# Kernel optimization log

Measured on AMD Instinct MI355X. Metric: run time of the kernel, lower is better.

The kernel has to match this reference:

```python
import jax, jax.numpy as jnp
import numpy as np

MAX_LANES = 5
DELTA_V = 1.0
DELTA_D = 6.0


def setup_inputs() -> dict:
    key = jax.random.key(0)
    k1, k2 = jax.random.split(key)
    targets = jax.random.randint(k1, (32, 360, 640), 0, 6, dtype=jnp.int32)
    embedding_vector = jax.random.normal(k2, (32, 4, 360, 640), dtype=jnp.float32)
    return {"targets": targets, "embedding_vector": embedding_vector}


def reference(targets, embedding_vector):
    B, C, H, W = embedding_vector.shape
    L = MAX_LANES
    P = H * W
    t = targets.reshape(B, P)                      # [B,P] labels 0..L
    e = embedding_vector.reshape(B, C, P)          # [B,C,P]

    # per-(batch, lane) segment counts and means
    onehot = (t[:, None, :] == jnp.arange(1, L + 1, dtype=t.dtype)[None, :, None])  # [B,L,P]
    counts = onehot.sum(-1)                        # [B,L] int
    valid = counts > 1                             # lane used only if >1 points
    sums = jnp.einsum('blp,bcp->blc', onehot.astype(e.dtype), e)   # [B,L,C]
    means = sums / jnp.maximum(counts, 1)[..., None].astype(e.dtype)  # [B,L,C]

    # ---- variance (pull) loss: per-point distance to its lane mean ----
    means_ext = jnp.concatenate([jnp.zeros((B, 1, C), e.dtype), means], axis=1)  # [B,L+1,C]
    mean_pix = jnp.take_along_axis(means_ext, t[..., None].astype(jnp.int32), axis=1)  # [B,P,C]
    diff = e.transpose(0, 2, 1) - mean_pix         # [B,P,C]
    sq = jnp.sum(diff * diff, axis=-1)             # [B,P]
    dist = jnp.sqrt(jnp.maximum(sq, 1e-12))
    valid_ext = jnp.concatenate([jnp.zeros((B, 1), bool), valid], axis=1)  # [B,L+1]
    pix_valid = jnp.take_along_axis(valid_ext, t.astype(jnp.int32), axis=1)  # [B,P]
    hinge = jax.nn.relu(dist - DELTA_V)
    dist_sum = jnp.sum(jnp.where(pix_valid, hinge * hinge, 0.0))
    point_count = jnp.sum(jnp.where(valid, counts, 0)).astype(e.dtype)
    dist_loss = jnp.where(point_count > 0, dist_sum / jnp.maximum(point_count, 1.0), 0.0)

    # ---- distance (push) loss: pdist over valid lane means per batch ----
    d = means[:, :, None, :] - means[:, None, :, :]          # [B,L,L,C]
    psq = jnp.sum(d * d, axis=-1)                            # [B,L,L]
    pd = jnp.sqrt(jnp.maximum(psq, 1e-12))
    iu = jnp.arange(L)
    pair_mask = valid[:, :, None] & valid[:, None, :] & (iu[:, None] < iu[None, :])  # [B,L,L]
    ph = jax.nn.relu(DELTA_D - pd)
    per_batch_sum = jnp.sum(jnp.where(pair_mask, ph * ph, 0.0), axis=(1, 2))  # [B]
    npairs = pair_mask.sum((1, 2)).astype(e.dtype)           # [B]
    batch_has = npairs > 0                                   # needs >=2 valid lanes
    var_b = jnp.where(batch_has, per_batch_sum / jnp.maximum(npairs, 1.0), 0.0)
    n_batches = batch_has.sum().astype(e.dtype)
    var_loss = jnp.where(n_batches > 0, var_b.sum() / jnp.maximum(n_batches, 1.0), 0.0)

    return dist_loss + var_loss
```

## Files before the change

### kernel.cpp

```cpp
#include <hip/hip_runtime.h>
#include <math.h>

#define B 32
#define C 4
#define H 360
#define W 640
#define P (H*W)
#define L 5
#define DELTA_V 1.0f
#define DELTA_D 6.0f

#define NV 25
#define BLK1 64
#define NBLK (B*BLK1)
#define G4 (P/4)

__device__ __forceinline__ float waveReduce(float v) {
#pragma unroll
    for (int off = 32; off; off >>= 1) v += __shfl_down(v, off, 64);
    return v;
}

__global__ __launch_bounds__(256) void seg_sums_k(const int* __restrict__ tgt,
                                                  const float* __restrict__ emb,
                                                  float* __restrict__ part1) {
    const int b = blockIdx.y;
    float s[L][C];
    float cn[L];
#pragma unroll
    for (int l = 0; l < L; ++l) {
        cn[l] = 0.f;
#pragma unroll
        for (int c = 0; c < C; ++c) s[l][c] = 0.f;
    }

    const int4*   t4 = (const int4*)(tgt + (size_t)b * P);
    const float4* e0 = (const float4*)(emb + (size_t)(b*C + 0) * P);
    const float4* e1 = (const float4*)(emb + (size_t)(b*C + 1) * P);
    const float4* e2 = (const float4*)(emb + (size_t)(b*C + 2) * P);
    const float4* e3 = (const float4*)(emb + (size_t)(b*C + 3) * P);

    auto proc = [&](int tt, float x0, float x1, float x2, float x3) {
#pragma unroll
        for (int l = 0; l < L; ++l) {
            float m = (tt == l + 1) ? 1.0f : 0.0f;
            cn[l] += m;
            s[l][0] = fmaf(m, x0, s[l][0]);
            s[l][1] = fmaf(m, x1, s[l][1]);
            s[l][2] = fmaf(m, x2, s[l][2]);
            s[l][3] = fmaf(m, x3, s[l][3]);
        }
    };

    for (int g = blockIdx.x * 256 + threadIdx.x; g < G4; g += BLK1 * 256) {
        int4   t  = t4[g];
        float4 a0 = e0[g], a1 = e1[g], a2 = e2[g], a3 = e3[g];
        proc(t.x, a0.x, a1.x, a2.x, a3.x);
        proc(t.y, a0.y, a1.y, a2.y, a3.y);
        proc(t.z, a0.z, a1.z, a2.z, a3.z);
        proc(t.w, a0.w, a1.w, a2.w, a3.w);
    }

    float vals[NV];
#pragma unroll
    for (int l = 0; l < L; ++l) {
#pragma unroll
        for (int c = 0; c < C; ++c) vals[l*4 + c] = s[l][c];
        vals[20 + l] = cn[l];
    }

    __shared__ float red[4][NV];
    const int lane = threadIdx.x & 63, wave = threadIdx.x >> 6;
#pragma unroll
    for (int k = 0; k < NV; ++k) {
        float r = waveReduce(vals[k]);
        if (lane == 0) red[wave][k] = r;
    }
    __syncthreads();
    if (threadIdx.x < NV) {
        float r = red[0][threadIdx.x] + red[1][threadIdx.x]
                + red[2][threadIdx.x] + red[3][threadIdx.x];
        part1[(size_t)(b * BLK1 + blockIdx.x) * NV + threadIdx.x] = r;
    }
}

__global__ __launch_bounds__(256) void means_k(const float* __restrict__ part1,
                                               float* __restrict__ means,
                                               float* __restrict__ validf,
                                               float* __restrict__ cntv) {
    const int seg  = (blockIdx.x * 256 + threadIdx.x) >> 6;
    const int lane = threadIdx.x & 63;
    if (seg >= B * L) return;
    const int b = seg / L, l = seg % L;

    const float* p = part1 + (size_t)(b * BLK1 + lane) * NV;
    float v0 = p[l*4+0], v1 = p[l*4+1], v2 = p[l*4+2], v3 = p[l*4+3], vc = p[20+l];
    v0 = waveReduce(v0); v1 = waveReduce(v1); v2 = waveReduce(v2);
    v3 = waveReduce(v3); vc = waveReduce(vc);
    if (lane == 0) {
        const float inv = 1.0f / fmaxf(vc, 1.0f);
        const bool  v   = vc > 1.5f;
        means[seg*4+0] = v0 * inv;
        means[seg*4+1] = v1 * inv;
        means[seg*4+2] = v2 * inv;
        means[seg*4+3] = v3 * inv;
        validf[seg] = v ? 1.f : 0.f;
        cntv[seg]   = v ? vc  : 0.f;
    }
}

__global__ __launch_bounds__(256) void pull_k(const int* __restrict__ tgt,
                                              const float* __restrict__ emb,
                                              const float* __restrict__ means,
                                              const float* __restrict__ validf,
                                              float* __restrict__ part3) {
    __shared__ float4 lmean[L + 1];
    __shared__ float  lvalid[L + 1];
    __shared__ float  lred[4];
    const int b = blockIdx.y;
    const int tid = threadIdx.x;

    if (tid == 0) { lmean[0] = make_float4(0.f, 0.f, 0.f, 0.f); lvalid[0] = 0.f; }
    else if (tid <= L) {
        lmean[tid]  = *(const float4*)(means + ((size_t)b*L + (tid-1)) * C);
        lvalid[tid] = validf[b*L + (tid-1)];
    }
    __syncthreads();

    const int4*   t4 = (const int4*)(tgt + (size_t)b * P);
    const float4* e0 = (const float4*)(emb + (size_t)(b*C + 0) * P);
    const float4* e1 = (const float4*)(emb + (size_t)(b*C + 1) * P);
    const float4* e2 = (const float4*)(emb + (size_t)(b*C + 2) * P);
    const float4* e3 = (const float4*)(emb + (size_t)(b*C + 3) * P);

    float acc = 0.f;
    auto proc = [&](int tt, float x0, float x1, float x2, float x3) {
        float4 m = lmean[tt];
        float d0 = x0 - m.x, d1 = x1 - m.y, d2 = x2 - m.z, d3 = x3 - m.w;
        float sq   = d0*d0 + d1*d1 + d2*d2 + d3*d3;
        float dist = sqrtf(fmaxf(sq, 1e-12f));
        float h    = fmaxf(dist - DELTA_V, 0.f);
        acc = fmaf(lvalid[tt] * h, h, acc);
    };

    for (int g = blockIdx.x * 256 + threadIdx.x; g < G4; g += BLK1 * 256) {
        int4   t  = t4[g];
        float4 a0 = e0[g], a1 = e1[g], a2 = e2[g], a3 = e3[g];
        proc(t.x, a0.x, a1.x, a2.x, a3.x);
        proc(t.y, a0.y, a1.y, a2.y, a3.y);
        proc(t.z, a0.z, a1.z, a2.z, a3.z);
        proc(t.w, a0.w, a1.w, a2.w, a3.w);
    }

    float r = waveReduce(acc);
    const int lane = tid & 63, wave = tid >> 6;
    if (lane == 0) lred[wave] = r;
    __syncthreads();
    if (tid == 0)
        part3[b * BLK1 + blockIdx.x] = lred[0] + lred[1] + lred[2] + lred[3];
}

__global__ __launch_bounds__(256) void finish_k(const float* __restrict__ part3,
                                                const float* __restrict__ means,
                                                const float* __restrict__ validf,
                                                const float* __restrict__ cntv,
                                                float* __restrict__ out) {
    __shared__ float red[4][4];
    const int tid = threadIdx.x;
    const int lane = tid & 63, wave = tid >> 6;

    float vb = 0.f, has = 0.f;
    if (tid < B) {
        const float* mb = means  + tid * L * 4;
        const float* vv = validf + tid * L;
        float ssum = 0.f, np = 0.f;
#pragma unroll
        for (int i = 0; i < L; ++i)
#pragma unroll
            for (int j = i + 1; j < L; ++j) {
                float ok = vv[i] * vv[j];
                float d0 = mb[i*4+0] - mb[j*4+0];
                float d1 = mb[i*4+1] - mb[j*4+1];
                float d2 = mb[i*4+2] - mb[j*4+2];
                float d3 = mb[i*4+3] - mb[j*4+3];
                float psq = d0*d0 + d1*d1 + d2*d2 + d3*d3;
                float pd  = sqrtf(fmaxf(psq, 1e-12f));
                float ph  = fmaxf(DELTA_D - pd, 0.f);
                ssum += ok * ph * ph;
                np   += ok;
            }
        if (np > 0.f) { vb = ssum / np; has = 1.f; }
    }
    float pc = (tid < B*L) ? cntv[tid] : 0.f;
    float ps = 0.f;
    for (int i = tid; i < NBLK; i += 256) ps += part3[i];

    float rvb = waveReduce(vb);
    float rhs = waveReduce(has);
    float rpc = waveReduce(pc);
    float rps = waveReduce(ps);
    if (lane == 0) { red[wave][0]=rvb; red[wave][1]=rhs; red[wave][2]=rpc; red[wave][3]=rps; }
    __syncthreads();
    if (tid == 0) {
        float svb = red[0][0]+red[1][0]+red[2][0]+red[3][0];
        float shs = red[0][1]+red[1][1]+red[2][1]+red[3][1];
        float spc = red[0][2]+red[1][2]+red[2][2]+red[3][2];
        float sps = red[0][3]+red[1][3]+red[2][3]+red[3][3];
        float var = (shs > 0.f) ? svb / shs : 0.f;
        float dl  = (spc > 0.f) ? sps / fmaxf(spc, 1.f) : 0.f;
        out[0] = dl + var;
    }
}

extern "C" void kernel_launch(void* const* d_in, const int* in_sizes, int n_in,
                              void* d_out, int out_size, void* d_ws, size_t ws_size,
                              hipStream_t stream) {
    const int*   tgt = (const int*)d_in[0];
    const float* emb = (const float*)d_in[1];

    float* ws     = (float*)d_ws;
    float* part1  = ws;
    float* means  = part1 + (size_t)NBLK * NV;
    float* validf = means + B*L*C;
    float* cntv   = validf + B*L;
    float* part3  = cntv + B*L;

    dim3 grid(BLK1, B);
    seg_sums_k<<<grid, 256, 0, stream>>>(tgt, emb, part1);
    means_k<<<(B*L + 3) / 4, 256, 0, stream>>>(part1, means, validf, cntv);
    pull_k<<<grid, 256, 0, stream>>>(tgt, emb, means, validf, part3);
    finish_k<<<1, 256, 0, stream>>>(part3, means, validf, cntv, (float*)d_out);
}
```

Measured before the change: 226.0 us.

## Use contiguous per-block chunks with register double-buffered prefetch in both streaming kernels

Each block now handles one contiguous chunk of the image instead of a grid-strided range, and the grid drops to 30 blocks per batch. Loads are software-pipelined through three register stages so the next tiles are in flight while the current one is processed, and a masked tail stage covers the remainder. The launch bounds ask for 4 blocks per SM. The intent is more memory-level parallelism in the bandwidth-bound passes, at the cost of higher register pressure and fewer blocks overall.

```diff
diff --git a/kernel.cpp b/kernel.cpp
--- a/kernel.cpp
+++ b/kernel.cpp
@@ -3,17 +3,17 @@
 
 #define B 32
 #define C 4
-#define H 360
-#define W 640
-#define P (H*W)
+#define P (360*640)
 #define L 5
 #define DELTA_V 1.0f
 #define DELTA_D 6.0f
 
 #define NV 25
-#define BLK1 64
+#define BLK1 30
 #define NBLK (B*BLK1)
 #define G4 (P/4)
+#define CHUNK_G (G4/BLK1)
+#define ITERS ((CHUNK_G + 255)/256)
 
 __device__ __forceinline__ float waveReduce(float v) {
 #pragma unroll
@@ -21,18 +21,14 @@
     return v;
 }
 
-__global__ __launch_bounds__(256) void seg_sums_k(const int* __restrict__ tgt,
-                                                  const float* __restrict__ emb,
-                                                  float* __restrict__ part1) {
-    const int b = blockIdx.y;
-    float s[L][C];
-    float cn[L];
-#pragma unroll
-    for (int l = 0; l < L; ++l) {
-        cn[l] = 0.f;
-#pragma unroll
-        for (int c = 0; c < C; ++c) s[l][c] = 0.f;
-    }
+struct Stage { int4 t; float4 a0, a1, a2, a3; };
+
+__global__ __launch_bounds__(256, 4) void seg_sums_k(const int* __restrict__ tgt,
+                                                     const float* __restrict__ emb,
+                                                     float* __restrict__ part1) {
+    const int b   = blockIdx.y;
+    const int tid = threadIdx.x;
+    const int gbase = blockIdx.x * CHUNK_G;
 
     const int4*   t4 = (const int4*)(tgt + (size_t)b * P);
     const float4* e0 = (const float4*)(emb + (size_t)(b*C + 0) * P);
@@ -40,7 +36,29 @@
     const float4* e2 = (const float4*)(emb + (size_t)(b*C + 2) * P);
     const float4* e3 = (const float4*)(emb + (size_t)(b*C + 3) * P);
 
-    auto proc = [&](int tt, float x0, float x1, float x2, float x3) {
+    float s[L][C], cn[L];
+#pragma unroll
+    for (int l = 0; l < L; ++l) { cn[l]=0.f; s[l][0]=s[l][1]=s[l][2]=s[l][3]=0.f; }
+
+    auto load_full = [&](int it) {
+        Stage st;
+        const int g = gbase + it*256 + tid;
+        st.t = t4[g];
+        st.a0 = e0[g]; st.a1 = e1[g]; st.a2 = e2[g]; st.a3 = e3[g];
+        return st;
+    };
+    auto load_tail = [&](int it) {
+        Stage st;
+        const int off = it*256 + tid;
+        const bool v  = off < CHUNK_G;
+        const int g   = gbase + (v ? off : 0);
+        st.t = t4[g];
+        st.a0 = e0[g]; st.a1 = e1[g]; st.a2 = e2[g]; st.a3 = e3[g];
+        if (!v) { st.t.x = 0; st.t.y = 0; st.t.z = 0; st.t.w = 0; }
+        return st;
+    };
+
+    auto proc1 = [&](int tt, float x0, float x1, float x2, float x3) {
 #pragma unroll
         for (int l = 0; l < L; ++l) {
             float m = (tt == l + 1) ? 1.0f : 0.0f;
@@ -51,15 +69,25 @@
             s[l][3] = fmaf(m, x3, s[l][3]);
         }
     };
-
-    for (int g = blockIdx.x * 256 + threadIdx.x; g < G4; g += BLK1 * 256) {
-        int4   t  = t4[g];
-        float4 a0 = e0[g], a1 = e1[g], a2 = e2[g], a3 = e3[g];
-        proc(t.x, a0.x, a1.x, a2.x, a3.x);
-        proc(t.y, a0.y, a1.y, a2.y, a3.y);
-        proc(t.z, a0.z, a1.z, a2.z, a3.z);
-        proc(t.w, a0.w, a1.w, a2.w, a3.w);
-    }
+    auto procS = [&](const Stage& st) {
+        proc1(st.t.x, st.a0.x, st.a1.x, st.a2.x, st.a3.x);
+        proc1(st.t.y, st.a0.y, st.a1.y, st.a2.y, st.a3.y);
+        proc1(st.t.z, st.a0.z, st.a1.z, st.a2.z, st.a3.z);
+        proc1(st.t.w, st.a0.w, st.a1.w, st.a2.w, st.a3.w);
+    };
+
+    Stage sA = load_full(0);
+    Stage sB = load_full(1);
+#pragma unroll
+    for (int it = 0; it < ITERS - 3; ++it) {
+        Stage sC = load_full(it + 2);
+        procS(sA);
+        sA = sB; sB = sC;
+    }
+    Stage sC = load_tail(ITERS - 1);
+    procS(sA);
+    procS(sB);
+    procS(sC);
 
     float vals[NV];
 #pragma unroll
@@ -68,19 +96,17 @@
         for (int c = 0; c < C; ++c) vals[l*4 + c] = s[l][c];
         vals[20 + l] = cn[l];
     }
-
     __shared__ float red[4][NV];
-    const int lane = threadIdx.x & 63, wave = threadIdx.x >> 6;
+    const int lane = tid & 63, wave = tid >> 6;
 #pragma unroll
     for (int k = 0; k < NV; ++k) {
         float r = waveReduce(vals[k]);
         if (lane == 0) red[wave][k] = r;
     }
     __syncthreads();
-    if (threadIdx.x < NV) {
-        float r = red[0][threadIdx.x] + red[1][threadIdx.x]
-                + red[2][threadIdx.x] + red[3][threadIdx.x];
-        part1[(size_t)(b * BLK1 + blockIdx.x) * NV + threadIdx.x] = r;
+    if (tid < NV) {
+        float r = red[0][tid] + red[1][tid] + red[2][tid] + red[3][tid];
+        part1[(size_t)(b * BLK1 + blockIdx.x) * NV + tid] = r;
     }
 }
 
@@ -93,8 +119,11 @@
     if (seg >= B * L) return;
     const int b = seg / L, l = seg % L;
 
-    const float* p = part1 + (size_t)(b * BLK1 + lane) * NV;
-    float v0 = p[l*4+0], v1 = p[l*4+1], v2 = p[l*4+2], v3 = p[l*4+3], vc = p[20+l];
+    float v0=0.f, v1=0.f, v2=0.f, v3=0.f, vc=0.f;
+    if (lane < BLK1) {
+        const float* p = part1 + (size_t)(b * BLK1 + lane) * NV;
+        v0 = p[l*4+0]; v1 = p[l*4+1]; v2 = p[l*4+2]; v3 = p[l*4+3]; vc = p[20+l];
+    }
     v0 = waveReduce(v0); v1 = waveReduce(v1); v2 = waveReduce(v2);
     v3 = waveReduce(v3); vc = waveReduce(vc);
     if (lane == 0) {
@@ -109,16 +138,17 @@
     }
 }
 
-__global__ __launch_bounds__(256) void pull_k(const int* __restrict__ tgt,
-                                              const float* __restrict__ emb,
-                                              const float* __restrict__ means,
-                                              const float* __restrict__ validf,
-                                              float* __restrict__ part3) {
+__global__ __launch_bounds__(256, 4) void pull_k(const int* __restrict__ tgt,
+                                                 const float* __restrict__ emb,
+                                                 const float* __restrict__ means,
+                                                 const float* __restrict__ validf,
+                                                 float* __restrict__ part3) {
     __shared__ float4 lmean[L + 1];
     __shared__ float  lvalid[L + 1];
     __shared__ float  lred[4];
-    const int b = blockIdx.y;
+    const int b   = blockIdx.y;
     const int tid = threadIdx.x;
+    const int gbase = blockIdx.x * CHUNK_G;
 
     if (tid == 0) { lmean[0] = make_float4(0.f, 0.f, 0.f, 0.f); lvalid[0] = 0.f; }
     else if (tid <= L) {
@@ -133,8 +163,26 @@
     const float4* e2 = (const float4*)(emb + (size_t)(b*C + 2) * P);
     const float4* e3 = (const float4*)(emb + (size_t)(b*C + 3) * P);
 
+    auto load_full = [&](int it) {
+        Stage st;
+        const int g = gbase + it*256 + tid;
+        st.t = t4[g];
+        st.a0 = e0[g]; st.a1 = e1[g]; st.a2 = e2[g]; st.a3 = e3[g];
+        return st;
+    };
+    auto load_tail = [&](int it) {
+        Stage st;
+        const int off = it*256 + tid;
+        const bool v  = off < CHUNK_G;
+        const int g   = gbase + (v ? off : 0);
+        st.t = t4[g];
+        st.a0 = e0[g]; st.a1 = e1[g]; st.a2 = e2[g]; st.a3 = e3[g];
+        if (!v) { st.t.x = 0; st.t.y = 0; st.t.z = 0; st.t.w = 0; }
+        return st;
+    };
+
     float acc = 0.f;
-    auto proc = [&](int tt, float x0, float x1, float x2, float x3) {
+    auto proc1 = [&](int tt, float x0, float x1, float x2, float x3) {
         float4 m = lmean[tt];
         float d0 = x0 - m.x, d1 = x1 - m.y, d2 = x2 - m.z, d3 = x3 - m.w;
         float sq   = d0*d0 + d1*d1 + d2*d2 + d3*d3;
@@ -142,15 +190,25 @@
         float h    = fmaxf(dist - DELTA_V, 0.f);
         acc = fmaf(lvalid[tt] * h, h, acc);
     };
-
-    for (int g = blockIdx.x * 256 + threadIdx.x; g < G4; g += BLK1 * 256) {
-        int4   t  = t4[g];
-        float4 a0 = e0[g], a1 = e1[g], a2 = e2[g], a3 = e3[g];
-        proc(t.x, a0.x, a1.x, a2.x, a3.x);
-        proc(t.y, a0.y, a1.y, a2.y, a3.y);
-        proc(t.z, a0.z, a1.z, a2.z, a3.z);
-        proc(t.w, a0.w, a1.w, a2.w, a3.w);
-    }
+    auto procS = [&](const Stage& st) {
+        proc1(st.t.x, st.a0.x, st.a1.x, st.a2.x, st.a3.x);
+        proc1(st.t.y, st.a0.y, st.a1.y, st.a2.y, st.a3.y);
+        proc1(st.t.z, st.a0.z, st.a1.z, st.a2.z, st.a3.z);
+        proc1(st.t.w, st.a0.w, st.a1.w, st.a2.w, st.a3.w);
+    };
+
+    Stage sA = load_full(0);
+    Stage sB = load_full(1);
+#pragma unroll
+    for (int it = 0; it < ITERS - 3; ++it) {
+        Stage sC = load_full(it + 2);
+        procS(sA);
+        sA = sB; sB = sC;
+    }
+    Stage sC = load_tail(ITERS - 1);
+    procS(sA);
+    procS(sB);
+    procS(sC);
 
     float r = waveReduce(acc);
     const int lane = tid & 63, wave = tid >> 6;
```

New measurement: 433.4 us. 1.92x slower.

## Split segment-sum kernel per channel with exact-fit grid and software-prefetched pull loop

Applied to the files above, without the earlier changes.

The segment-sum kernel now runs one block per (chunk, channel, batch), so each thread keeps only 10 accumulators instead of 25. All of its loads are issued up front over a fixed five-iteration tiling (45 blocks x 5 x 256 = P/4 exactly). The pull kernel uses the same exact-fit tiling and double-buffers its loads so the next tile's reads overlap the current compute. The cost is that targets are re-read once per channel (4x target traffic) in the first pass, and the code now relies on P dividing evenly with no bounds checks.

```diff
diff --git a/kernel.cpp b/kernel.cpp
--- a/kernel.cpp
+++ b/kernel.cpp
@@ -3,17 +3,15 @@
 
 #define B 32
 #define C 4
-#define H 360
-#define W 640
-#define P (H*W)
+#define P (360*640)
 #define L 5
 #define DELTA_V 1.0f
 #define DELTA_D 6.0f
 
-#define NV 25
-#define BLK1 64
-#define NBLK (B*BLK1)
+#define BLKX 45
+#define ITER1 5
 #define G4 (P/4)
+#define NBLK3 (B*BLKX)
 
 __device__ __forceinline__ float waveReduce(float v) {
 #pragma unroll
@@ -21,70 +19,68 @@
     return v;
 }
 
-__global__ __launch_bounds__(256) void seg_sums_k(const int* __restrict__ tgt,
-                                                  const float* __restrict__ emb,
-                                                  float* __restrict__ part1) {
-    const int b = blockIdx.y;
-    float s[L][C];
-    float cn[L];
-#pragma unroll
-    for (int l = 0; l < L; ++l) {
-        cn[l] = 0.f;
-#pragma unroll
-        for (int c = 0; c < C; ++c) s[l][c] = 0.f;
-    }
+__global__ __launch_bounds__(256, 4) void seg_sums_k(const int* __restrict__ tgt,
+                                                     const float* __restrict__ emb,
+                                                     float* __restrict__ sums,
+                                                     float* __restrict__ cnts) {
+    const int x = blockIdx.x, c = blockIdx.y, b = blockIdx.z;
+    const int tid = threadIdx.x;
 
     const int4*   t4 = (const int4*)(tgt + (size_t)b * P);
-    const float4* e0 = (const float4*)(emb + (size_t)(b*C + 0) * P);
-    const float4* e1 = (const float4*)(emb + (size_t)(b*C + 1) * P);
-    const float4* e2 = (const float4*)(emb + (size_t)(b*C + 2) * P);
-    const float4* e3 = (const float4*)(emb + (size_t)(b*C + 3) * P);
-
-    auto proc = [&](int tt, float x0, float x1, float x2, float x3) {
+    const float4* ec = (const float4*)(emb + ((size_t)b * C + c) * P);
+
+    int4   tv[ITER1];
+    float4 ev[ITER1];
+#pragma unroll
+    for (int it = 0; it < ITER1; ++it) {
+        const int g = (x + it * BLKX) * 256 + tid;
+        tv[it] = t4[g];
+        ev[it] = ec[g];
+    }
+
+    float s[L], n[L];
+#pragma unroll
+    for (int l = 0; l < L; ++l) { s[l] = 0.f; n[l] = 0.f; }
+
+    auto acc1 = [&](int tt, float e) {
 #pragma unroll
         for (int l = 0; l < L; ++l) {
             float m = (tt == l + 1) ? 1.0f : 0.0f;
-            cn[l] += m;
-            s[l][0] = fmaf(m, x0, s[l][0]);
-            s[l][1] = fmaf(m, x1, s[l][1]);
-            s[l][2] = fmaf(m, x2, s[l][2]);
-            s[l][3] = fmaf(m, x3, s[l][3]);
+            n[l] += m;
+            s[l] = fmaf(m, e, s[l]);
         }
     };
-
-    for (int g = blockIdx.x * 256 + threadIdx.x; g < G4; g += BLK1 * 256) {
-        int4   t  = t4[g];
-        float4 a0 = e0[g], a1 = e1[g], a2 = e2[g], a3 = e3[g];
-        proc(t.x, a0.x, a1.x, a2.x, a3.x);
-        proc(t.y, a0.y, a1.y, a2.y, a3.y);
-        proc(t.z, a0.z, a1.z, a2.z, a3.z);
-        proc(t.w, a0.w, a1.w, a2.w, a3.w);
-    }
-
-    float vals[NV];
-#pragma unroll
-    for (int l = 0; l < L; ++l) {
-#pragma unroll
-        for (int c = 0; c < C; ++c) vals[l*4 + c] = s[l][c];
-        vals[20 + l] = cn[l];
-    }
-
-    __shared__ float red[4][NV];
-    const int lane = threadIdx.x & 63, wave = threadIdx.x >> 6;
-#pragma unroll
-    for (int k = 0; k < NV; ++k) {
+#pragma unroll
+    for (int it = 0; it < ITER1; ++it) {
+        acc1(tv[it].x, ev[it].x);
+        acc1(tv[it].y, ev[it].y);
+        acc1(tv[it].z, ev[it].z);
+        acc1(tv[it].w, ev[it].w);
+    }
+
+    float vals[2*L];
+#pragma unroll
+    for (int l = 0; l < L; ++l) { vals[l] = s[l]; vals[L + l] = n[l]; }
+
+    __shared__ float red[4][2*L];
+    const int lane = tid & 63, wave = tid >> 6;
+#pragma unroll
+    for (int k = 0; k < 2*L; ++k) {
         float r = waveReduce(vals[k]);
         if (lane == 0) red[wave][k] = r;
     }
     __syncthreads();
-    if (threadIdx.x < NV) {
-        float r = red[0][threadIdx.x] + red[1][threadIdx.x]
-                + red[2][threadIdx.x] + red[3][threadIdx.x];
-        part1[(size_t)(b * BLK1 + blockIdx.x) * NV + threadIdx.x] = r;
-    }
-}
-
-__global__ __launch_bounds__(256) void means_k(const float* __restrict__ part1,
+    if (tid < L) {
+        float r = red[0][tid] + red[1][tid] + red[2][tid] + red[3][tid];
+        sums[((size_t)(b * BLKX + x) * C + c) * L + tid] = r;
+    } else if (c == 0 && tid < 2*L) {
+        float r = red[0][tid] + red[1][tid] + red[2][tid] + red[3][tid];
+        cnts[(size_t)(b * BLKX + x) * L + (tid - L)] = r;
+    }
+}
+
+__global__ __launch_bounds__(256) void means_k(const float* __restrict__ sums,
+                                               const float* __restrict__ cnts,
                                                float* __restrict__ means,
                                                float* __restrict__ validf,
                                                float* __restrict__ cntv) {
@@ -93,8 +89,15 @@
     if (seg >= B * L) return;
     const int b = seg / L, l = seg % L;
 
-    const float* p = part1 + (size_t)(b * BLK1 + lane) * NV;
-    float v0 = p[l*4+0], v1 = p[l*4+1], v2 = p[l*4+2], v3 = p[l*4+3], vc = p[20+l];
+    float v0=0.f, v1=0.f, v2=0.f, v3=0.f, vc=0.f;
+    if (lane < BLKX) {
+        const size_t base = (size_t)(b * BLKX + lane) * C * L;
+        v0 = sums[base + 0*L + l];
+        v1 = sums[base + 1*L + l];
+        v2 = sums[base + 2*L + l];
+        v3 = sums[base + 3*L + l];
+        vc = cnts[(size_t)(b * BLKX + lane) * L + l];
+    }
     v0 = waveReduce(v0); v1 = waveReduce(v1); v2 = waveReduce(v2);
     v3 = waveReduce(v3); vc = waveReduce(vc);
     if (lane == 0) {
@@ -109,55 +112,65 @@
     }
 }
 
-__global__ __launch_bounds__(256) void pull_k(const int* __restrict__ tgt,
-                                              const float* __restrict__ emb,
-                                              const float* __restrict__ means,
-                                              const float* __restrict__ validf,
-                                              float* __restrict__ part3) {
+__global__ __launch_bounds__(256, 4) void pull_k(const int* __restrict__ tgt,
+                                                 const float* __restrict__ emb,
+                                                 const float* __restrict__ means,
+                                                 const float* __restrict__ validf,
+                                                 float* __restrict__ part3) {
     __shared__ float4 lmean[L + 1];
     __shared__ float  lvalid[L + 1];
     __shared__ float  lred[4];
-    const int b = blockIdx.y;
+    const int x = blockIdx.x, b = blockIdx.y;
     const int tid = threadIdx.x;
 
     if (tid == 0) { lmean[0] = make_float4(0.f, 0.f, 0.f, 0.f); lvalid[0] = 0.f; }
     else if (tid <= L) {
-        lmean[tid]  = *(const float4*)(means + ((size_t)b*L + (tid-1)) * C);
+        lmean[tid]  = *(const float4*)(means + ((size_t)b*L + (tid-1)) * 4);
         lvalid[tid] = validf[b*L + (tid-1)];
     }
     __syncthreads();
 
     const int4*   t4 = (const int4*)(tgt + (size_t)b * P);
-    const float4* e0 = (const float4*)(emb + (size_t)(b*C + 0) * P);
-    const float4* e1 = (const float4*)(emb + (size_t)(b*C + 1) * P);
-    const float4* e2 = (const float4*)(emb + (size_t)(b*C + 2) * P);
-    const float4* e3 = (const float4*)(emb + (size_t)(b*C + 3) * P);
+    const float4* e0 = (const float4*)(emb + ((size_t)b*C + 0) * P);
+    const float4* e1 = (const float4*)(emb + ((size_t)b*C + 1) * P);
+    const float4* e2 = (const float4*)(emb + ((size_t)b*C + 2) * P);
+    const float4* e3 = (const float4*)(emb + ((size_t)b*C + 3) * P);
 
     float acc = 0.f;
-    auto proc = [&](int tt, float x0, float x1, float x2, float x3) {
+    auto proc1 = [&](int tt, float v0, float v1, float v2, float v3) {
         float4 m = lmean[tt];
-        float d0 = x0 - m.x, d1 = x1 - m.y, d2 = x2 - m.z, d3 = x3 - m.w;
+        float d0 = v0 - m.x, d1 = v1 - m.y, d2 = v2 - m.z, d3 = v3 - m.w;
         float sq   = d0*d0 + d1*d1 + d2*d2 + d3*d3;
         float dist = sqrtf(fmaxf(sq, 1e-12f));
         float h    = fmaxf(dist - DELTA_V, 0.f);
         acc = fmaf(lvalid[tt] * h, h, acc);
     };
 
-    for (int g = blockIdx.x * 256 + threadIdx.x; g < G4; g += BLK1 * 256) {
-        int4   t  = t4[g];
-        float4 a0 = e0[g], a1 = e1[g], a2 = e2[g], a3 = e3[g];
-        proc(t.x, a0.x, a1.x, a2.x, a3.x);
-        proc(t.y, a0.y, a1.y, a2.y, a3.y);
-        proc(t.z, a0.z, a1.z, a2.z, a3.z);
-        proc(t.w, a0.w, a1.w, a2.w, a3.w);
-    }
+    int g = x * 256 + tid;
+    int4   ta = t4[g];
+    float4 p0 = e0[g], p1 = e1[g], p2 = e2[g], p3 = e3[g];
+#pragma unroll
+    for (int it = 0; it < ITER1 - 1; ++it) {
+        const int gn = (x + (it + 1) * BLKX) * 256 + tid;
+        int4   tb = t4[gn];
+        float4 q0 = e0[gn], q1 = e1[gn], q2 = e2[gn], q3 = e3[gn];
+        proc1(ta.x, p0.x, p1.x, p2.x, p3.x);
+        proc1(ta.y, p0.y, p1.y, p2.y, p3.y);
+        proc1(ta.z, p0.z, p1.z, p2.z, p3.z);
+        proc1(ta.w, p0.w, p1.w, p2.w, p3.w);
+        ta = tb; p0 = q0; p1 = q1; p2 = q2; p3 = q3;
+    }
+    proc1(ta.x, p0.x, p1.x, p2.x, p3.x);
+    proc1(ta.y, p0.y, p1.y, p2.y, p3.y);
+    proc1(ta.z, p0.z, p1.z, p2.z, p3.z);
+    proc1(ta.w, p0.w, p1.w, p2.w, p3.w);
 
     float r = waveReduce(acc);
     const int lane = tid & 63, wave = tid >> 6;
     if (lane == 0) lred[wave] = r;
     __syncthreads();
     if (tid == 0)
-        part3[b * BLK1 + blockIdx.x] = lred[0] + lred[1] + lred[2] + lred[3];
+        part3[b * BLKX + x] = lred[0] + lred[1] + lred[2] + lred[3];
 }
 
 __global__ __launch_bounds__(256) void finish_k(const float* __restrict__ part3,
@@ -193,7 +206,7 @@
     }
     float pc = (tid < B*L) ? cntv[tid] : 0.f;
     float ps = 0.f;
-    for (int i = tid; i < NBLK; i += 256) ps += part3[i];
+    for (int i = tid; i < NBLK3; i += 256) ps += part3[i];
 
     float rvb = waveReduce(vb);
     float rhs = waveReduce(has);
@@ -219,15 +232,15 @@
     const float* emb = (const float*)d_in[1];
 
     float* ws     = (float*)d_ws;
-    float* part1  = ws;
-    float* means  = part1 + (size_t)NBLK * NV;
-    float* validf = means + B*L*C;
+    float* sums   = ws;
+    float* cnts   = sums + (size_t)B*BLKX*C*L;
+    float* means  = cnts + (size_t)B*BLKX*L;
+    float* validf = means + B*L*4;
     float* cntv   = validf + B*L;
     float* part3  = cntv + B*L;
 
-    dim3 grid(BLK1, B);
-    seg_sums_k<<<grid, 256, 0, stream>>>(tgt, emb, part1);
-    means_k<<<(B*L + 3) / 4, 256, 0, stream>>>(part1, means, validf, cntv);
-    pull_k<<<grid, 256, 0, stream>>>(tgt, emb, means, validf, part3);
+    seg_sums_k<<<dim3(BLKX, C, B), 256, 0, stream>>>(tgt, emb, sums, cnts);
+    means_k<<<(B*L + 3) / 4, 256, 0, stream>>>(sums, cnts, means, validf, cntv);
+    pull_k<<<dim3(BLKX, B), 256, 0, stream>>>(tgt, emb, means, validf, part3);
     finish_k<<<1, 256, 0, stream>>>(part3, means, validf, cntv, (float*)d_out);
 }
```

Result: faster. 218.6 us (-3.3%).
